# Optimization experiments

Measured on AMD Instinct MI355X. Metric: run time of the kernel, lower is better.

## Reference

```python
import jax, jax.numpy as jnp
import numpy as np

V = 30000    # vocab_size
E = 128      # embedding_dim
ENC = 128    # encode_dim
H = 128      # hidden_dim
B = 64       # batch of programs
S = 32       # statements per program (max_len)
K = 64       # AST nodes per statement tree
T = B * S    # statement trees per side
N = T * K    # AST nodes per side
LEVELS = 8   # >= max tree depth (heap layout depth = 6)


def setup_inputs() -> dict:
    key = jax.random.key(0)
    ks = jax.random.split(key, 10)
    # heap-structured trees: node j's parent is (j-1)//2 within its K-node tree
    j = np.tile(np.arange(K), T)
    start = np.repeat(np.arange(T) * K, K)
    parent = np.where(j == 0, N, start + (j - 1) // 2).astype(np.int32)  # roots -> dummy slot N

    def rn(k, shape, scale):
        return jax.random.normal(k, shape, dtype=jnp.float32) * scale

    return {
        "tokens1": jax.random.randint(ks[0], (N,), 0, V, dtype=jnp.int32),
        "parent1": jnp.asarray(parent),
        "tokens2": jax.random.randint(ks[1], (N,), 0, V, dtype=jnp.int32),
        "parent2": jnp.asarray(parent),
        "emb": rn(ks[2], (V, E), 1.0),
        "w_c": rn(ks[3], (ENC, E), E ** -0.5),
        "b_c": jnp.zeros((ENC,), jnp.float32),
        "w_ih_f": rn(ks[4], (3 * H, ENC), ENC ** -0.5),
        "w_hh_f": rn(ks[5], (3 * H, H), H ** -0.5),
        "b_ih_f": jnp.zeros((3 * H,), jnp.float32),
        "b_hh_f": jnp.zeros((3 * H,), jnp.float32),
        "w_ih_b": rn(ks[6], (3 * H, ENC), ENC ** -0.5),
        "w_hh_b": rn(ks[7], (3 * H, H), H ** -0.5),
        "b_ih_b": jnp.zeros((3 * H,), jnp.float32),
        "b_hh_b": jnp.zeros((3 * H,), jnp.float32),
        "w_out": rn(ks[8], (1, H), H ** -0.5),
        "b_out": jnp.zeros((1,), jnp.float32),
    }


def _tree_encode(tokens, parent, emb, w_c, b_c):
    # per-node projection: W_c(embedding(token))  (no activation, as in source)
    base = emb[tokens] @ w_c.T + b_c              # [N, ENC]
    h = base
    for _ in range(LEVELS):                        # level-synchronous subtree sums
        child = jax.ops.segment_sum(h, parent, num_segments=N + 1)[:N]
        h = base + child                           # h_v = base_v + sum_children h_c
    tree_id = jnp.arange(N) // K
    res = jax.ops.segment_max(h, tree_id, num_segments=T)  # [T, ENC]
    return jnp.maximum(res, 0.0)                   # zeros in batch_node join the max


def _gru_scan(xs, h0, w_ih, w_hh, b_ih, b_hh):
    # torch nn.GRU cell math
    def step(h, x_t):
        gi = x_t @ w_ih.T + b_ih
        gh = h @ w_hh.T + b_hh
        i_r, i_z, i_n = jnp.split(gi, 3, axis=-1)
        h_r, h_z, h_n = jnp.split(gh, 3, axis=-1)
        r = jax.nn.sigmoid(i_r + h_r)
        z = jax.nn.sigmoid(i_z + h_z)
        n = jnp.tanh(i_n + r * h_n)
        return (1.0 - z) * n + z * h, None
    h_fin, _ = jax.lax.scan(step, h0, xs)
    return h_fin


def _encode(tokens, parent, emb, w_c, b_c,
            w_ih_f, w_hh_f, b_ih_f, b_hh_f, w_ih_b, w_hh_b, b_ih_b, b_hh_b):
    seq = _tree_encode(tokens, parent, emb, w_c, b_c).reshape(B, S, ENC)
    xs = jnp.transpose(seq, (1, 0, 2))  # [S, B, ENC]
    h0 = jnp.zeros((B, H), seq.dtype)
    hf = _gru_scan(xs, h0, w_ih_f, w_hh_f, b_ih_f, b_hh_f)
    hb = _gru_scan(xs[::-1], h0, w_ih_b, w_hh_b, b_ih_b, b_hh_b)
    return hf + hb                       # pooled program representation [B, H]


def reference(tokens1, parent1, tokens2, parent2, emb, w_c, b_c,
              w_ih_f, w_hh_f, b_ih_f, b_hh_f, w_ih_b, w_hh_b, b_ih_b, b_hh_b,
              w_out, b_out):
    gp = (w_ih_f, w_hh_f, b_ih_f, b_hh_f, w_ih_b, w_hh_b, b_ih_b, b_hh_b)
    lvec = _encode(tokens1, parent1, emb, w_c, b_c, *gp)
    rvec = _encode(tokens2, parent2, emb, w_c, b_c, *gp)
    dist = jnp.abs(lvec - rvec)
    return jax.nn.sigmoid(dist @ w_out.T + b_out)  # [B, 1]
```

## Files before the change

### kernel.cpp

```cpp
#include <hip/hip_runtime.h>
#include <stdint.h>

#define VSZ 30000
#define TPS 2048
#define G3  384

#define OFF_PROJ   0u
#define OFF_SEQ    1920000u
#define OFF_HFIN   2444288u
#define OFF_FRAG   2477056u

using f32x4 = __attribute__((ext_vector_type(4))) float;
using s16x8 = __attribute__((ext_vector_type(8))) short;
union U8 { uint4 u; s16x8 s; };

__device__ __forceinline__ float sigm(float x) { return 1.0f / (1.0f + __expf(-x)); }
__device__ __forceinline__ float tanh_fast(float x) {
  float e = __expf(-2.0f * x);
  return 2.0f / (1.0f + e) - 1.0f;
}
__device__ __forceinline__ unsigned bf16_rn(float f) {
  unsigned u = __float_as_uint(f);
  return (u + 0x7FFFu + ((u >> 16) & 1u)) >> 16;
}

#define KT 1040
#define XS 4160
#define MM(dst, A, B) dst = __builtin_amdgcn_mfma_f32_16x16x32_bf16(A, B, dst, 0, 0, 0)

__global__ __launch_bounds__(256) void k_pack(
    const float* __restrict__ w_ih_f, const float* __restrict__ w_ih_b,
    const float* __restrict__ w_hh_f, const float* __restrict__ w_hh_b,
    uint4* __restrict__ fragimg) {
  int idx = blockIdx.x * 256 + threadIdx.x;
  int l = idx & 63;
  int t = (idx >> 6) & 3;
  int r = idx >> 8;
  int g = r % 3; r /= 3;
  int mat = r & 1; r >>= 1;
  int w = r & 7;
  int dir = r >> 3;
  const float* src = mat ? (dir ? w_hh_b : w_hh_f) : (dir ? w_ih_b : w_ih_f);
  int row = g * 128 + 16 * w + (l & 15);
  int ks  = t * 32 + (l >> 4) * 8;
  float4 f0 = *(const float4*)&src[row * 128 + ks];
  float4 f1 = *(const float4*)&src[row * 128 + ks + 4];
  uint4 u;
  u.x = bf16_rn(f0.x) | (bf16_rn(f0.y) << 16);
  u.y = bf16_rn(f0.z) | (bf16_rn(f0.w) << 16);
  u.z = bf16_rn(f1.x) | (bf16_rn(f1.y) << 16);
  u.w = bf16_rn(f1.z) | (bf16_rn(f1.w) << 16);
  fragimg[idx] = u;
}

__global__ __launch_bounds__(512) void k_proj(const float* __restrict__ emb,
                                              const float* __restrict__ w_c,
                                              const float* __restrict__ b_c,
                                              unsigned short* __restrict__ projb) {
  __shared__ __align__(16) char blds[8 * XS];
  int tid = threadIdx.x;
  int v0 = blockIdx.x * 128;
  {
    int pp = tid >> 5, cc = tid & 31;
    int wbyte = (cc >> 3) * KT + (pp + 16 * ((cc & 7) >> 1)) * 16 + (cc & 1) * 8;
    for (int nt = 0; nt < 8; ++nt) {
      int row = v0 + nt * 16 + pp;
      float4 v = make_float4(0.f, 0.f, 0.f, 0.f);
      if (row < VSZ) v = *(const float4*)&emb[(size_t)row * 128 + 4 * cc];
      uint2 u;
      u.x = bf16_rn(v.x) | (bf16_rn(v.y) << 16);
      u.y = bf16_rn(v.z) | (bf16_rn(v.w) << 16);
      *(uint2*)(blds + nt * XS + wbyte) = u;
    }
  }
  int w = tid >> 6, l = tid & 63;
  s16x8 af[4];
  {
    int row = 16 * w + (l & 15);
    int kb = (l >> 4) * 8;
#pragma unroll
    for (int t = 0; t < 4; ++t) {
      float4 f0 = *(const float4*)&w_c[row * 128 + t * 32 + kb];
      float4 f1 = *(const float4*)&w_c[row * 128 + t * 32 + kb + 4];
      U8 u;
      u.u.x = bf16_rn(f0.x) | (bf16_rn(f0.y) << 16);
      u.u.y = bf16_rn(f0.z) | (bf16_rn(f0.w) << 16);
      u.u.z = bf16_rn(f1.x) | (bf16_rn(f1.y) << 16);
      u.u.w = bf16_rn(f1.z) | (bf16_rn(f1.w) << 16);
      af[t] = u.s;
    }
  }
  f32x4 bias = *(const f32x4*)&b_c[16 * w + (l >> 4) * 4];
  __syncthreads();
  for (int nt = 0; nt < 8; ++nt) {
    s16x8 bf[4];
#pragma unroll
    for (int t = 0; t < 4; ++t) {
      U8 u; u.u = *(const uint4*)(blds + nt * XS + t * KT + l * 16);
      bf[t] = u.s;
    }
    f32x4 acc = bias;
    MM(acc, af[0], bf[0]); MM(acc, af[1], bf[1]);
    MM(acc, af[2], bf[2]); MM(acc, af[3], bf[3]);
    int v = v0 + nt * 16 + (l & 15);
    if (v < VSZ) {
      uint2 u;
      u.x = bf16_rn(acc[0]) | (bf16_rn(acc[1]) << 16);
      u.y = bf16_rn(acc[2]) | (bf16_rn(acc[3]) << 16);
      *(uint2*)&projb[(size_t)v * 128 + 16 * w + (l >> 4) * 4] = u;
    }
  }
}

__global__ __launch_bounds__(512) void k_tree(const int* __restrict__ tokens1,
                                              const int* __restrict__ tokens2,
                                              const unsigned short* __restrict__ projb,
                                              float* __restrict__ seq) {
  __shared__ int tok[4][64];
  int side = blockIdx.y;
  const int* tokens = side ? tokens2 : tokens1;
  int t0 = blockIdx.x * 4;
  if (threadIdx.x < 256) {
    int tl = threadIdx.x >> 6, j = threadIdx.x & 63;
    tok[tl][j] = tokens[(t0 + tl) * 64 + j];
  }
  __syncthreads();
  int tl = threadIdx.x >> 7;
  int c  = threadIdx.x & 127;
  float s[64];
#pragma unroll
  for (int j = 0; j < 64; ++j)
    s[j] = __uint_as_float(((unsigned)projb[(size_t)tok[tl][j] * 128 + c]) << 16);
  s[31] += s[63];
#pragma unroll
  for (int j = 30; j >= 0; --j) s[j] += s[2 * j + 1] + s[2 * j + 2];
  float m = s[0];
#pragma unroll
  for (int j = 1; j < 64; ++j) m = fmaxf(m, s[j]);
  m = fmaxf(m, 0.0f);
  seq[(size_t)(side * TPS + t0 + tl) * 128 + c] = m;
}

__global__ __launch_bounds__(512) void k_scan(
    const float* __restrict__ seq,
    const uint4* __restrict__ fragimg,
    const float* __restrict__ b_ih_f, const float* __restrict__ b_ih_b,
    const float* __restrict__ b_hh_f, const float* __restrict__ b_hh_b,
    float* __restrict__ hfin) {
  __shared__ __align__(16) uint4 wlds[6144];
  __shared__ __align__(16) char  xlds[8 * XS];
  __shared__ __align__(16) unsigned hbuf[2][1040];
  int bx = blockIdx.x;
  int sd = bx & 3, pg = bx >> 2;
  int side = sd >> 1, dir = sd & 1;
  const float* bih = dir ? b_ih_b : b_ih_f;
  const float* bhh = dir ? b_hh_b : b_hh_f;
  int tid = threadIdx.x;
  int w = tid >> 6, l = tid & 63;
  int p  = l & 15;
  int kb = l >> 4;
  int c0 = 16 * w + 4 * kb;

  for (int i = tid; i < 6144; i += 512) {
    int w_ = i / 768, r = i - w_ * 768;
    wlds[i] = fragimg[(size_t)(dir * 8 + w_) * 1536 + 768 + r];
  }
  for (int i = tid; i < 2080; i += 512) ((unsigned*)hbuf)[i] = 0u;

  int pp = tid >> 5, cc = tid & 31;
  int xwb = (cc >> 3) * KT + (pp + 16 * ((cc & 7) >> 1)) * 16 + (cc & 1) * 8;
  const float* srow = seq + (size_t)(side * TPS + (pg * 16 + pp) * 32) * 128 + 4 * cc;
#pragma unroll
  for (int ss = 0; ss < 8; ++ss) {
    int pos = dir ? (31 - ss) : ss;
    float4 v = *(const float4*)(srow + (size_t)pos * 128);
    uint2 u;
    u.x = bf16_rn(v.x) | (bf16_rn(v.y) << 16);
    u.y = bf16_rn(v.z) | (bf16_rn(v.w) << 16);
    *(uint2*)(xlds + ss * XS + xwb) = u;
  }

  const uint4* fbase = fragimg + (size_t)(dir * 8 + w) * 1536 + l;
  s16x8 ai[3][4];
#pragma unroll
  for (int g = 0; g < 3; ++g)
#pragma unroll
    for (int t = 0; t < 4; ++t) {
      U8 u; u.u = fbase[g * 256 + t * 64];
      ai[g][t] = u.s;
    }

  f32x4 bir = *(const f32x4*)&bih[c0],       bhr = *(const f32x4*)&bhh[c0];
  f32x4 biz = *(const f32x4*)&bih[128 + c0], bhz = *(const f32x4*)&bhh[128 + c0];
  f32x4 bin = *(const f32x4*)&bih[256 + c0], bhn = *(const f32x4*)&bhh[256 + c0];
  f32x4 bbr = bir + bhr, bbz = biz + bhz;

  int hwb = (c0 >> 5) * KT + (p + 16 * ((c0 & 31) >> 3)) * 16 + (c0 & 7) * 2;
  const uint4* wbase = wlds + w * 768 + l;

  float hc[4] = {0.f, 0.f, 0.f, 0.f};
  f32x4 z4 = {0.f, 0.f, 0.f, 0.f};
  __syncthreads();

  for (int i = 0; i < 32; ++i) {
    if (i && (i & 7) == 0) {
#pragma unroll
      for (int ss = 0; ss < 8; ++ss) {
        int pos = dir ? (31 - (i + ss)) : (i + ss);
        float4 v = *(const float4*)(srow + (size_t)pos * 128);
        uint2 u;
        u.x = bf16_rn(v.x) | (bf16_rn(v.y) << 16);
        u.y = bf16_rn(v.z) | (bf16_rn(v.w) << 16);
        *(uint2*)(xlds + ss * XS + xwb) = u;
      }
      __syncthreads();
    }
    const char* xb = xlds + (i & 7) * XS;
    const char* hb = (const char*)hbuf + (i & 1) * 4160;
    s16x8 xf[4], bf[4];
#pragma unroll
    for (int t = 0; t < 4; ++t) {
      U8 ux; ux.u = *(const uint4*)(xb + t * KT + l * 16); xf[t] = ux.s;
      U8 uh; uh.u = *(const uint4*)(hb + t * KT + l * 16); bf[t] = uh.s;
    }
    f32x4 aR0 = bbr, aR1 = z4, aZ0 = bbz, aZ1 = z4;
    f32x4 aNi0 = bin, aNi1 = z4, aNh0 = bhn, aNh1 = z4;
    MM(aR0,  ai[0][0], xf[0]); MM(aZ0,  ai[1][0], xf[0]); MM(aNi0, ai[2][0], xf[0]);
    MM(aR1,  ai[0][1], xf[1]); MM(aZ1,  ai[1][1], xf[1]); MM(aNi1, ai[2][1], xf[1]);
    MM(aR0,  ai[0][2], xf[2]); MM(aZ0,  ai[1][2], xf[2]); MM(aNi0, ai[2][2], xf[2]);
    MM(aR1,  ai[0][3], xf[3]); MM(aZ1,  ai[1][3], xf[3]); MM(aNi1, ai[2][3], xf[3]);
#pragma unroll
    for (int t = 0; t < 4; ++t) {
      U8 u0, u1, u2;
      u0.u = wbase[t * 64];
      u1.u = wbase[(4 + t) * 64];
      u2.u = wbase[(8 + t) * 64];
      if (t & 1) { MM(aR1, u0.s, bf[t]); MM(aZ1, u1.s, bf[t]); MM(aNh1, u2.s, bf[t]); }
      else       { MM(aR0, u0.s, bf[t]); MM(aZ0, u1.s, bf[t]); MM(aNh0, u2.s, bf[t]); }
    }
#pragma unroll
    for (int r4 = 0; r4 < 4; ++r4) {
      float rv = sigm(aR0[r4] + aR1[r4]);
      float zv = sigm(aZ0[r4] + aZ1[r4]);
      float nv = tanh_fast(aNi0[r4] + aNi1[r4] + rv * (aNh0[r4] + aNh1[r4]));
      hc[r4] = (1.0f - zv) * nv + zv * hc[r4];
    }
    uint2 hp;
    hp.x = bf16_rn(hc[0]) | (bf16_rn(hc[1]) << 16);
    hp.y = bf16_rn(hc[2]) | (bf16_rn(hc[3]) << 16);
    *(uint2*)((char*)hbuf + ((i + 1) & 1) * 4160 + hwb) = hp;
    __syncthreads();
  }
  int scan = sd * 64 + pg * 16 + p;
#pragma unroll
  for (int r4 = 0; r4 < 4; ++r4)
    hfin[(size_t)scan * 128 + c0 + r4] = hc[r4];
}

__global__ __launch_bounds__(64) void k_out(const float* __restrict__ hfin,
                                            const float* __restrict__ w_out,
                                            const float* __restrict__ b_out,
                                            float* __restrict__ out) {
  int b = blockIdx.x, lane = threadIdx.x;
  float p = 0.f;
#pragma unroll
  for (int i = 0; i < 2; ++i) {
    int c = lane + i * 64;
    float l = hfin[(size_t)(0   + b) * 128 + c] + hfin[(size_t)(64  + b) * 128 + c];
    float r = hfin[(size_t)(128 + b) * 128 + c] + hfin[(size_t)(192 + b) * 128 + c];
    p += fabsf(l - r) * w_out[c];
  }
#pragma unroll
  for (int off = 32; off > 0; off >>= 1) p += __shfl_down(p, off);
  if (lane == 0) out[b] = sigm(p + b_out[0]);
}

extern "C" void kernel_launch(void* const* d_in, const int* in_sizes, int n_in,
                              void* d_out, int out_size, void* d_ws, size_t ws_size,
                              hipStream_t stream) {
  (void)in_sizes; (void)n_in; (void)out_size; (void)ws_size;
  const int*   tokens1 = (const int*)d_in[0];
  const int*   tokens2 = (const int*)d_in[2];
  const float* emb     = (const float*)d_in[4];
  const float* w_c     = (const float*)d_in[5];
  const float* b_c     = (const float*)d_in[6];
  const float* w_ih_f  = (const float*)d_in[7];
  const float* w_hh_f  = (const float*)d_in[8];
  const float* b_ih_f  = (const float*)d_in[9];
  const float* b_hh_f  = (const float*)d_in[10];
  const float* w_ih_b  = (const float*)d_in[11];
  const float* w_hh_b  = (const float*)d_in[12];
  const float* b_ih_b  = (const float*)d_in[13];
  const float* b_hh_b  = (const float*)d_in[14];
  const float* w_out   = (const float*)d_in[15];
  const float* b_out   = (const float*)d_in[16];
  float* ws = (float*)d_ws;
  unsigned short* projb = (unsigned short*)(ws + OFF_PROJ);
  float* seq    = ws + OFF_SEQ;
  float* hfin   = ws + OFF_HFIN;
  uint4* fragimg = (uint4*)(ws + OFF_FRAG);

  k_pack<<<96, 256, 0, stream>>>(w_ih_f, w_ih_b, w_hh_f, w_hh_b, fragimg);
  k_proj<<<(VSZ + 127) / 128, 512, 0, stream>>>(emb, w_c, b_c, projb);
  k_tree<<<dim3(TPS / 4, 2), 512, 0, stream>>>(tokens1, tokens2, projb, seq);
  k_scan<<<16, 512, 0, stream>>>(seq, fragimg, b_ih_f, b_ih_b, b_hh_f, b_hh_b, hfin);
  k_out<<<64, 64, 0, stream>>>(hfin, w_out, b_out, (float*)d_out);
}
```

Measured before the change: 99.02 us.

## Use raw LDS barriers, reload input weights per step, hardware bf16 pack

In the GRU scan kernel, each __syncthreads is replaced by an LDS-only wait (lgkmcnt) plus s_barrier and a sched_barrier. Outstanding global loads can therefore stay in flight across the per-step barrier. The input-weight fragments are no longer held in registers for the whole scan; they are re-fetched from global memory after the input MFMAs, acting as a prefetch for the next step. The kernel gets a (512,2) launch bound to cap register use. Software bf16 rounding is replaced by v_cvt_pk_bf16_f32, which shortens the serial per-step critical path but adds a global load every iteration and relies on hand-placed waits for correctness.

```diff
diff --git a/kernel.cpp b/kernel.cpp
--- a/kernel.cpp
+++ b/kernel.cpp
@@ -141,7 +141,7 @@
   seq[(size_t)(side * TPS + t0 + tl) * 128 + c] = m;
 }
 
-__global__ __launch_bounds__(512) void k_scan(
+__global__ __launch_bounds__(512, 2) void k_scan(
     const float* __restrict__ seq,
     const uint4* __restrict__ fragimg,
     const float* __restrict__ b_ih_f, const float* __restrict__ b_ih_b,
@@ -181,14 +181,12 @@
   }
 
   const uint4* fbase = fragimg + (size_t)(dir * 8 + w) * 1536 + l;
-  s16x8 ai[3][4];
+  s16x8 aiP[3][4];
 #pragma unroll
   for (int g = 0; g < 3; ++g)
 #pragma unroll
-    for (int t = 0; t < 4; ++t) {
-      U8 u; u.u = fbase[g * 256 + t * 64];
-      ai[g][t] = u.s;
-    }
+    for (int t = 0; t < 4; ++t)
+      aiP[g][t] = *(const s16x8*)&fbase[g * 256 + t * 64];
 
   f32x4 bir = *(const f32x4*)&bih[c0],       bhr = *(const f32x4*)&bhh[c0];
   f32x4 biz = *(const f32x4*)&bih[128 + c0], bhz = *(const f32x4*)&bhh[128 + c0];
@@ -213,30 +211,40 @@
         u.y = bf16_rn(v.z) | (bf16_rn(v.w) << 16);
         *(uint2*)(xlds + ss * XS + xwb) = u;
       }
-      __syncthreads();
+      asm volatile("s_waitcnt lgkmcnt(0)" ::: "memory");
+      __builtin_amdgcn_s_barrier();
+      __builtin_amdgcn_sched_barrier(0);
     }
     const char* xb = xlds + (i & 7) * XS;
     const char* hb = (const char*)hbuf + (i & 1) * 4160;
     s16x8 xf[4], bf[4];
 #pragma unroll
     for (int t = 0; t < 4; ++t) {
-      U8 ux; ux.u = *(const uint4*)(xb + t * KT + l * 16); xf[t] = ux.s;
-      U8 uh; uh.u = *(const uint4*)(hb + t * KT + l * 16); bf[t] = uh.s;
+      xf[t] = *(const s16x8*)(xb + t * KT + l * 16);
+      bf[t] = *(const s16x8*)(hb + t * KT + l * 16);
     }
     f32x4 aR0 = bbr, aR1 = z4, aZ0 = bbz, aZ1 = z4;
     f32x4 aNi0 = bin, aNi1 = z4, aNh0 = bhn, aNh1 = z4;
-    MM(aR0,  ai[0][0], xf[0]); MM(aZ0,  ai[1][0], xf[0]); MM(aNi0, ai[2][0], xf[0]);
-    MM(aR1,  ai[0][1], xf[1]); MM(aZ1,  ai[1][1], xf[1]); MM(aNi1, ai[2][1], xf[1]);
-    MM(aR0,  ai[0][2], xf[2]); MM(aZ0,  ai[1][2], xf[2]); MM(aNi0, ai[2][2], xf[2]);
-    MM(aR1,  ai[0][3], xf[3]); MM(aZ1,  ai[1][3], xf[3]); MM(aNi1, ai[2][3], xf[3]);
+    MM(aR0,  aiP[0][0], xf[0]); MM(aZ0,  aiP[1][0], xf[0]); MM(aNi0, aiP[2][0], xf[0]);
+    MM(aR1,  aiP[0][1], xf[1]); MM(aZ1,  aiP[1][1], xf[1]); MM(aNi1, aiP[2][1], xf[1]);
+    MM(aR0,  aiP[0][2], xf[2]); MM(aZ0,  aiP[1][2], xf[2]); MM(aNi0, aiP[2][2], xf[2]);
+    MM(aR1,  aiP[0][3], xf[3]); MM(aZ1,  aiP[1][3], xf[3]); MM(aNi1, aiP[2][3], xf[3]);
+    {
+      const uint4* fb = fbase;
+      asm volatile("" : "+v"(fb));
+#pragma unroll
+      for (int g = 0; g < 3; ++g)
+#pragma unroll
+        for (int t = 0; t < 4; ++t)
+          aiP[g][t] = *(const s16x8*)&fb[g * 256 + t * 64];
+    }
 #pragma unroll
     for (int t = 0; t < 4; ++t) {
-      U8 u0, u1, u2;
-      u0.u = wbase[t * 64];
-      u1.u = wbase[(4 + t) * 64];
-      u2.u = wbase[(8 + t) * 64];
-      if (t & 1) { MM(aR1, u0.s, bf[t]); MM(aZ1, u1.s, bf[t]); MM(aNh1, u2.s, bf[t]); }
-      else       { MM(aR0, u0.s, bf[t]); MM(aZ0, u1.s, bf[t]); MM(aNh0, u2.s, bf[t]); }
+      s16x8 u0 = *(const s16x8*)&wbase[t * 64];
+      s16x8 u1 = *(const s16x8*)&wbase[(4 + t) * 64];
+      s16x8 u2 = *(const s16x8*)&wbase[(8 + t) * 64];
+      if (t & 1) { MM(aR1, u0, bf[t]); MM(aZ1, u1, bf[t]); MM(aNh1, u2, bf[t]); }
+      else       { MM(aR0, u0, bf[t]); MM(aZ0, u1, bf[t]); MM(aNh0, u2, bf[t]); }
     }
 #pragma unroll
     for (int r4 = 0; r4 < 4; ++r4) {
@@ -245,11 +253,14 @@
       float nv = tanh_fast(aNi0[r4] + aNi1[r4] + rv * (aNh0[r4] + aNh1[r4]));
       hc[r4] = (1.0f - zv) * nv + zv * hc[r4];
     }
-    uint2 hp;
-    hp.x = bf16_rn(hc[0]) | (bf16_rn(hc[1]) << 16);
-    hp.y = bf16_rn(hc[2]) | (bf16_rn(hc[3]) << 16);
+    unsigned hp0, hp1;
+    asm("v_cvt_pk_bf16_f32 %0, %1, %2" : "=v"(hp0) : "v"(hc[0]), "v"(hc[1]));
+    asm("v_cvt_pk_bf16_f32 %0, %1, %2" : "=v"(hp1) : "v"(hc[2]), "v"(hc[3]));
+    uint2 hp; hp.x = hp0; hp.y = hp1;
     *(uint2*)((char*)hbuf + ((i + 1) & 1) * 4160 + hwb) = hp;
-    __syncthreads();
+    asm volatile("s_waitcnt lgkmcnt(0)" ::: "memory");
+    __builtin_amdgcn_s_barrier();
+    __builtin_amdgcn_sched_barrier(0);
   }
   int scan = sd * 64 + pg * 16 + p;
 #pragma unroll
```

Measured after the change: 109.1 us. 1.1x slower.
